# Performance work log

Hardware: AMD Instinct MI355X
Metric: run time of the kernel (lower is better)

Reference implementation:

```python
import jax, jax.numpy as jnp
import numpy as np

DIM = 2048
INTER = 1408
N_EXPERTS = 16
TOP_K = 2
N_SHARED = 2
SHARED_INTER = N_SHARED * INTER  # 2816


def setup_inputs() -> dict:
    key = jax.random.key(0)
    ks = jax.random.split(key, 9)
    s = 0.02
    return {
        "x": jax.random.normal(ks[0], (4, 2048, DIM), dtype=jnp.float32),
        "gate_w": jax.random.normal(ks[1], (N_EXPERTS, DIM), dtype=jnp.float32) * s,
        "w1": jax.random.normal(ks[2], (N_EXPERTS, INTER, DIM), dtype=jnp.float32) * s,
        "w2": jax.random.normal(ks[3], (N_EXPERTS, DIM, INTER), dtype=jnp.float32) * s,
        "w3": jax.random.normal(ks[4], (N_EXPERTS, INTER, DIM), dtype=jnp.float32) * s,
        "sw1": jax.random.normal(ks[5], (SHARED_INTER, DIM), dtype=jnp.float32) * s,
        "sw2": jax.random.normal(ks[6], (DIM, SHARED_INTER), dtype=jnp.float32) * s,
        "sw3": jax.random.normal(ks[7], (SHARED_INTER, DIM), dtype=jnp.float32) * s,
    }


def _swiglu(t, wa, wb, wo):
    # t: [T, d_in]; wa, wb: [d_h, d_in]; wo: [d_out, d_h]
    h = jax.nn.silu(t @ wa.T) * (t @ wb.T)
    return h @ wo.T


def reference(x, gate_w, w1, w2, w3, sw1, sw2, sw3):
    shape = x.shape
    t = x.reshape(-1, DIM)                      # [T, dim]
    scores = jax.nn.softmax(t @ gate_w.T, axis=-1)  # [T, E]
    weights, indices = jax.lax.top_k(scores, TOP_K)  # [T, k] each

    y = jnp.zeros_like(t)
    # Small fixed loop over experts (structurally distinct weights).
    # Per-token combine weight for expert e: sum over top-k slots routed to e
    # (matches y[idx] += expert(x[idx]) * weights[idx, top]; zero weight for
    # unrouted tokens reproduces the counts[i]==0 skip exactly).
    for e in range(N_EXPERTS):
        w_e = jnp.sum(jnp.where(indices == e, weights, 0.0), axis=-1)  # [T]
        y = y + _swiglu(t, w1[e], w3[e], w2[e]) * w_e[:, None]

    z = _swiglu(t, sw1, sw3, sw2)               # shared experts MLP
    return (y + z).reshape(shape)
```

## Files before the change

kernel.cpp:

```cpp
#include <hip/hip_runtime.h>
#include <hip/hip_bf16.h>

#define DIM 2048
#define INTER 1408
#define NEXP 16
#define NTOK 8192
#define SINTER 2816

typedef __attribute__((ext_vector_type(8))) short bf16x8;
typedef __attribute__((ext_vector_type(4))) float f32x4;
typedef __attribute__((ext_vector_type(4))) unsigned short u16x4;
typedef __attribute__((ext_vector_type(8))) unsigned short u16x8;

#define VMCNT(n) asm volatile("s_waitcnt vmcnt(" #n ")" ::: "memory")
#define BARRIER() __builtin_amdgcn_s_barrier()
#define SCHEDB() __builtin_amdgcn_sched_barrier(0)

__device__ __forceinline__ unsigned short f2bf(float f) {
    union { float f; unsigned u; } a; a.f = f;
    unsigned r = a.u + 0x7fffu + ((a.u >> 16) & 1u);
    return (unsigned short)(r >> 16);
}

__device__ __forceinline__ void gload16(const void* g, void* lds) {
    __builtin_amdgcn_global_load_lds(
        (const __attribute__((address_space(1))) void*)g,
        (__attribute__((address_space(3))) void*)lds, 16, 0, 0);
}

__global__ __launch_bounds__(256) void cast_bf16(const float* __restrict__ s,
                                                 unsigned short* __restrict__ d,
                                                 long long n) {
    long long i = ((long long)blockIdx.x * 256 + threadIdx.x) * 8;
    if (i >= n) return;
    float4 a = *(const float4*)(s + i), b = *(const float4*)(s + i + 4);
    u16x8 o = { f2bf(a.x), f2bf(a.y), f2bf(a.z), f2bf(a.w),
                f2bf(b.x), f2bf(b.y), f2bf(b.z), f2bf(b.w) };
    *(u16x8*)(d + i) = o;
}

__global__ __launch_bounds__(256) void gate_topk(
    const float* __restrict__ x, const float* __restrict__ gw,
    unsigned short* __restrict__ xb,
    int* __restrict__ counts, int* __restrict__ toklist, float* __restrict__ tokw) {
    int wave = threadIdx.x >> 6;
    int lane = threadIdx.x & 63;
    int tok  = blockIdx.x * 4 + wave;
    const float* xr = x + (size_t)tok * DIM;
    unsigned short* xbr = xb + (size_t)tok * DIM;

    float part[NEXP];
#pragma unroll
    for (int e = 0; e < NEXP; ++e) part[e] = 0.f;
#pragma unroll
    for (int c = 0; c < DIM / 256; ++c) {
        float4 xv = *(const float4*)(xr + c * 256 + lane * 4);
        u16x4 xo = { f2bf(xv.x), f2bf(xv.y), f2bf(xv.z), f2bf(xv.w) };
        *(u16x4*)(xbr + c * 256 + lane * 4) = xo;
#pragma unroll
        for (int e = 0; e < NEXP; ++e) {
            float4 g = *(const float4*)(gw + e * DIM + c * 256 + lane * 4);
            part[e] += xv.x * g.x + xv.y * g.y + xv.z * g.z + xv.w * g.w;
        }
    }
#pragma unroll
    for (int e = 0; e < NEXP; ++e) {
        float v = part[e];
#pragma unroll
        for (int off = 32; off; off >>= 1) v += __shfl_xor(v, off);
        part[e] = v;
    }
    float mx = part[0];
#pragma unroll
    for (int e = 1; e < NEXP; ++e) mx = fmaxf(mx, part[e]);
    float Z = 0.f;
#pragma unroll
    for (int e = 0; e < NEXP; ++e) Z += expf(part[e] - mx);
    int i1 = 0; float m1 = part[0];
#pragma unroll
    for (int e = 1; e < NEXP; ++e) if (part[e] > m1) { m1 = part[e]; i1 = e; }
    int i2 = -1; float m2 = -1e30f;
#pragma unroll
    for (int e = 0; e < NEXP; ++e) if (e != i1 && part[e] > m2) { m2 = part[e]; i2 = e; }
    if (lane == 0) {
        float w1v = expf(m1 - mx) / Z;
        float w2v = expf(m2 - mx) / Z;
        int p1 = atomicAdd(&counts[i1], 1);
        toklist[i1 * NTOK + p1] = tok; tokw[i1 * NTOK + p1] = w1v;
        int p2 = atomicAdd(&counts[i2], 1);
        toklist[i2 * NTOK + p2] = tok; tokw[i2 * NTOK + p2] = w2v;
    }
}

__global__ void prefix_k(const int* __restrict__ counts, int* __restrict__ base) {
    if (threadIdx.x == 0) {
        int acc = 0;
        for (int e = 0; e < NEXP; ++e) { base[e] = acc; acc += counts[e]; }
        base[16] = acc;
        base[17] = acc + NTOK;
    }
}

__device__ __forceinline__ int swz(int r) { return (r ^ (r >> 2)) & 3; }

__global__ __launch_bounds__(512, 2) void gemm1(
    const unsigned short* __restrict__ xb,
    const unsigned short* __restrict__ w1b, const unsigned short* __restrict__ w3b,
    const unsigned short* __restrict__ sw1b, const unsigned short* __restrict__ sw3b,
    const int* __restrict__ counts, const int* __restrict__ base,
    const int* __restrict__ toklist, unsigned short* __restrict__ hbuf) {
    const int e   = blockIdx.z;
    const int cnt = (e < NEXP) ? counts[e] : NTOK;
    const int m0  = blockIdx.y * 256;
    if (m0 >= cnt) return;
    const int n0  = blockIdx.x * 128;
    const size_t woff = (size_t)((e < NEXP) ? e : e - NEXP) * INTER * DIM;
    const unsigned short* B1 = ((e < NEXP) ? w1b : sw1b) + woff;
    const unsigned short* B3 = ((e < NEXP) ? w3b : sw3b) + woff;
    const int hbase = base[e];
    const int* tl = toklist + e * NTOK;

    __shared__ __attribute__((aligned(16))) unsigned short As[4][8192];
    __shared__ __attribute__((aligned(16))) unsigned short B1s[4][4096];
    __shared__ __attribute__((aligned(16))) unsigned short B3s[4][4096];

    const int tid = threadIdx.x;
    const int w = tid >> 6, l = tid & 63;
    const int wr = w >> 1, wc = w & 1;
    const int lr = l & 15, hi = l >> 4;

    const int row0 = tid >> 2, row1 = row0 + 128;
    const int c0 = (tid & 3) ^ swz(row0);
    int g0 = m0 + row0, g1 = m0 + row1;
    int t0, t1;
    if (e < NEXP) { t0 = (g0 < cnt) ? tl[g0] : 0; t1 = (g1 < cnt) ? tl[g1] : 0; }
    else          { t0 = g0; t1 = g1; }
    const unsigned short* aSrc0 = xb + (size_t)t0 * DIM + c0 * 8;
    const unsigned short* aSrc1 = xb + (size_t)t1 * DIM + c0 * 8;
    const unsigned short* b1Src = B1 + (size_t)(n0 + row0) * DIM + c0 * 8;
    const unsigned short* b3Src = B3 + (size_t)(n0 + row0) * DIM + c0 * 8;

    int aoff[4], boff[4];
#pragma unroll
    for (int m = 0; m < 4; ++m) {
        int r = wr * 64 + m * 16 + lr;
        aoff[m] = r * 64 + ((swz(r) ^ hi) << 4);
    }
#pragma unroll
    for (int n = 0; n < 4; ++n) {
        int r = wc * 64 + n * 16 + lr;
        boff[n] = r * 64 + ((swz(r) ^ hi) << 4);
    }

    f32x4 acc1[4][4], acc3[4][4];
#pragma unroll
    for (int m = 0; m < 4; ++m)
#pragma unroll
        for (int n = 0; n < 4; ++n) {
            acc1[m][n] = (f32x4){0.f, 0.f, 0.f, 0.f};
            acc3[m][n] = (f32x4){0.f, 0.f, 0.f, 0.f};
        }

    const int H = DIM / 32;

    auto STAGE = [&](int hh) {
        int hb = hh & 3;
        int kc = hh * 32;
        gload16(aSrc0 + kc, &As[hb][tid * 8]);
        gload16(aSrc1 + kc, &As[hb][4096 + tid * 8]);
        gload16(b1Src + kc, &B1s[hb][tid * 8]);
        gload16(b3Src + kc, &B3s[hb][tid * 8]);
    };
    auto READF = [&](bf16x8 (&af)[4], bf16x8 (&b1)[4], bf16x8 (&b3)[4], int hh) {
        int hb = hh & 3;
        const char* As_ = (const char*)&As[hb][0];
        const char* B1_ = (const char*)&B1s[hb][0];
        const char* B3_ = (const char*)&B3s[hb][0];
#pragma unroll
        for (int m = 0; m < 4; ++m) af[m] = *(const bf16x8*)(As_ + aoff[m]);
#pragma unroll
        for (int n = 0; n < 4; ++n) {
            b1[n] = *(const bf16x8*)(B1_ + boff[n]);
            b3[n] = *(const bf16x8*)(B3_ + boff[n]);
        }
    };
    auto MMA = [&](bf16x8 (&af)[4], bf16x8 (&b1)[4], bf16x8 (&b3)[4]) {
        __builtin_amdgcn_s_setprio(1);
#pragma unroll
        for (int m = 0; m < 4; ++m)
#pragma unroll
            for (int n = 0; n < 4; ++n) {
                acc1[m][n] = __builtin_amdgcn_mfma_f32_16x16x32_bf16(af[m], b1[n], acc1[m][n], 0, 0, 0);
                acc3[m][n] = __builtin_amdgcn_mfma_f32_16x16x32_bf16(af[m], b3[n], acc3[m][n], 0, 0, 0);
            }
        __builtin_amdgcn_s_setprio(0);
    };

    bf16x8 afA[4], b1A[4], b3A[4], afB[4], b1B[4], b3B[4];

    STAGE(0); STAGE(1); STAGE(2);
    VMCNT(8);
    BARRIER();
    READF(afA, b1A, b3A, 0);

    for (int h = 0; h < H; h += 2) {
        if (h + 3 < H) { STAGE(h + 3); VMCNT(8); }
        else if (h == H - 2) { VMCNT(0); }
        BARRIER();
        READF(afB, b1B, b3B, h + 1);
        SCHEDB();
        MMA(afA, b1A, b3A);
        if (h + 4 < H) { STAGE(h + 4); VMCNT(8); }
        else if (h + 1 == H - 3) { VMCNT(4); }
        BARRIER();
        READF(afA, b1A, b3A, h + 2);
        SCHEDB();
        MMA(afB, b1B, b3B);
    }

#pragma unroll
    for (int m = 0; m < 4; ++m) {
#pragma unroll
        for (int i = 0; i < 4; ++i) {
            int row  = wr * 64 + m * 16 + hi * 4 + i;
            int grow = m0 + row;
            if (grow < cnt) {
                size_t ro = (size_t)(hbase + grow) * INTER;
#pragma unroll
                for (int n = 0; n < 4; ++n) {
                    int col = n0 + wc * 64 + n * 16 + lr;
                    float a = acc1[m][n][i];
                    float hv = a / (1.f + __expf(-a)) * acc3[m][n][i];
                    hbuf[ro + col] = f2bf(hv);
                }
            }
        }
    }
}

__global__ __launch_bounds__(512, 2) void gemm2(
    const unsigned short* __restrict__ hbuf,
    const unsigned short* __restrict__ w2b, const unsigned short* __restrict__ sw2b,
    const int* __restrict__ counts, const int* __restrict__ base,
    const int* __restrict__ toklist, const float* __restrict__ tokw,
    float* __restrict__ out) {
    const int e   = blockIdx.z;
    const int cnt = (e < NEXP) ? counts[e] : NTOK;
    const int m0  = blockIdx.y * 256;
    if (m0 >= cnt) return;
    const int n0  = blockIdx.x * 128;
    const int hbase = base[e];
    const size_t bstride = (e < NEXP) ? INTER : SINTER;
    const unsigned short* Bb = (e < NEXP) ? w2b + (size_t)e * DIM * INTER
                                          : sw2b + (size_t)(e - NEXP) * INTER;

    __shared__ __attribute__((aligned(16))) unsigned short Ah[4][8192];
    __shared__ __attribute__((aligned(16))) unsigned short Bh[4][4096];

    const int tid = threadIdx.x;
    const int w = tid >> 6, l = tid & 63;
    const int wr = w >> 1, wc = w & 1;
    const int lr = l & 15, hi = l >> 4;

    const int row0 = tid >> 2, row1 = row0 + 128;
    const int c0 = (tid & 3) ^ swz(row0);
    const unsigned short* aSrc0 = hbuf + (size_t)(hbase + m0 + row0) * INTER + c0 * 8;
    const unsigned short* aSrc1 = hbuf + (size_t)(hbase + m0 + row1) * INTER + c0 * 8;
    const unsigned short* bSrc  = Bb + (size_t)(n0 + row0) * bstride + c0 * 8;

    int aoff[4], boff[4];
#pragma unroll
    for (int m = 0; m < 4; ++m) {
        int r = wr * 64 + m * 16 + lr;
        aoff[m] = r * 64 + ((swz(r) ^ hi) << 4);
    }
#pragma unroll
    for (int n = 0; n < 4; ++n) {
        int r = wc * 64 + n * 16 + lr;
        boff[n] = r * 64 + ((swz(r) ^ hi) << 4);
    }

    f32x4 acc[4][4];
#pragma unroll
    for (int m = 0; m < 4; ++m)
#pragma unroll
        for (int n = 0; n < 4; ++n) acc[m][n] = (f32x4){0.f, 0.f, 0.f, 0.f};

    const int H = INTER / 32;

    auto STAGE = [&](int hh) {
        int hb = hh & 3;
        int kc = hh * 32;
        gload16(aSrc0 + kc, &Ah[hb][tid * 8]);
        gload16(aSrc1 + kc, &Ah[hb][4096 + tid * 8]);
        gload16(bSrc  + kc, &Bh[hb][tid * 8]);
    };
    auto READF = [&](bf16x8 (&af)[4], bf16x8 (&bf)[4], int hh) {
        int hb = hh & 3;
        const char* A_ = (const char*)&Ah[hb][0];
        const char* B_ = (const char*)&Bh[hb][0];
#pragma unroll
        for (int m = 0; m < 4; ++m) af[m] = *(const bf16x8*)(A_ + aoff[m]);
#pragma unroll
        for (int n = 0; n < 4; ++n) bf[n] = *(const bf16x8*)(B_ + boff[n]);
    };
    auto MMA = [&](bf16x8 (&af)[4], bf16x8 (&bf)[4]) {
        __builtin_amdgcn_s_setprio(1);
#pragma unroll
        for (int m = 0; m < 4; ++m)
#pragma unroll
            for (int n = 0; n < 4; ++n)
                acc[m][n] = __builtin_amdgcn_mfma_f32_16x16x32_bf16(af[m], bf[n], acc[m][n], 0, 0, 0);
        __builtin_amdgcn_s_setprio(0);
    };

    bf16x8 afA[4], bfA[4], afB[4], bfB[4];

    STAGE(0); STAGE(1); STAGE(2);
    VMCNT(6);
    BARRIER();
    READF(afA, bfA, 0);

    for (int h = 0; h < H; h += 2) {
        if (h + 3 < H) { STAGE(h + 3); VMCNT(6); }
        else if (h == H - 2) { VMCNT(0); }
        BARRIER();
        READF(afB, bfB, h + 1);
        SCHEDB();
        MMA(afA, bfA);
        if (h + 4 < H) { STAGE(h + 4); VMCNT(6); }
        else if (h + 1 == H - 3) { VMCNT(3); }
        BARRIER();
        READF(afA, bfA, h + 2);
        SCHEDB();
        MMA(afB, bfB);
    }

#pragma unroll
    for (int m = 0; m < 4; ++m) {
#pragma unroll
        for (int i = 0; i < 4; ++i) {
            int row  = wr * 64 + m * 16 + hi * 4 + i;
            int grow = m0 + row;
            if (grow < cnt) {
                int tok; float wt;
                if (e < NEXP) { tok = toklist[e * NTOK + grow]; wt = tokw[e * NTOK + grow]; }
                else          { tok = grow; wt = 1.f; }
                float* orow = out + (size_t)tok * DIM + n0 + wc * 64 + lr;
#pragma unroll
                for (int n = 0; n < 4; ++n)
                    unsafeAtomicAdd(orow + n * 16, acc[m][n][i] * wt);
            }
        }
    }
}

extern "C" void kernel_launch(void* const* d_in, const int* in_sizes, int n_in,
                              void* d_out, int out_size, void* d_ws, size_t ws_size,
                              hipStream_t stream) {
    const float* x   = (const float*)d_in[0];
    const float* gw  = (const float*)d_in[1];
    const float* w1  = (const float*)d_in[2];
    const float* w2  = (const float*)d_in[3];
    const float* w3  = (const float*)d_in[4];
    const float* sw1 = (const float*)d_in[5];
    const float* sw2 = (const float*)d_in[6];
    const float* sw3 = (const float*)d_in[7];
    float* out = (float*)d_out;

    char* ws = (char*)d_ws;
    int*   counts  = (int*)ws;
    int*   basep   = (int*)(ws + 128);
    int*   toklist = (int*)(ws + 4096);
    float* tokw    = (float*)(ws + 4096 + (size_t)NEXP * NTOK * 4);
    unsigned short* hbuf = (unsigned short*)(ws + (2u << 20));

    const size_t hbytes = (size_t)4 * NTOK * INTER * 2;
    const size_t offx   = (2ull << 20) + hbytes;
    const size_t xbytes = (size_t)NTOK * DIM * 2;
    const size_t offw   = offx + xbytes;
    const size_t wB     = (size_t)NEXP * INTER * DIM * 2;
    const size_t swB    = (size_t)SINTER * DIM * 2;

    unsigned short* xb   = (unsigned short*)(ws + offx);
    unsigned short* w1b  = (unsigned short*)(ws + offw);
    unsigned short* w3b  = (unsigned short*)(ws + offw + wB);
    unsigned short* w2b  = (unsigned short*)(ws + offw + 2 * wB);
    unsigned short* sw1b = (unsigned short*)(ws + offw + 3 * wB);
    unsigned short* sw3b = (unsigned short*)(ws + offw + 3 * wB + swB);
    unsigned short* sw2b = (unsigned short*)(ws + offw + 3 * wB + 2 * swB);

    hipMemsetAsync(counts, 0, 64, stream);
    hipMemsetAsync(d_out, 0, (size_t)out_size * sizeof(float), stream);

    gate_topk<<<NTOK / 4, 256, 0, stream>>>(x, gw, xb, counts, toklist, tokw);
    prefix_k<<<1, 64, 0, stream>>>(counts, basep);

    auto cast = [&](const float* s, unsigned short* d, long long n) {
        cast_bf16<<<(int)((n / 8 + 255) / 256), 256, 0, stream>>>(s, d, n);
    };
    cast(w1, w1b, (long long)NEXP * INTER * DIM);
    cast(w3, w3b, (long long)NEXP * INTER * DIM);
    cast(w2, w2b, (long long)NEXP * INTER * DIM);
    cast(sw1, sw1b, (long long)SINTER * DIM);
    cast(sw3, sw3b, (long long)SINTER * DIM);
    cast(sw2, sw2b, (long long)SINTER * DIM);

    gemm1<<<dim3(INTER / 128, NTOK / 256, 18), 512, 0, stream>>>(
        xb, w1b, w3b, sw1b, sw3b, counts, basep, toklist, hbuf);
    gemm2<<<dim3(DIM / 128, NTOK / 256, 18), 512, 0, stream>>>(
        hbuf, w2b, sw2b, counts, basep, toklist, tokw, out);
}
```

Baseline: 1.444 ms.

## Simplify GEMM pipelines to single-buffered register loop with prefetch distance two

Both GEMM main loops drop the unrolled A/B register double-buffering and the sched barriers. Each iteration now loads fragments from LDS, issues the global-to-LDS stage two tiles ahead (previously three), waits, then runs the MFMAs with the n loop outermost and the w1 and w3 products issued separately. This lowers register pressure and lets the compiler schedule freely, but exposes LDS read latency before the MFMAs and reduces prefetch depth. The w2 and sw2 weight casts now launch after gemm1 instead of before it.

```diff
diff --git a/kernel.cpp b/kernel.cpp
--- a/kernel.cpp
+++ b/kernel.cpp
@@ -14,7 +14,6 @@
 
 #define VMCNT(n) asm volatile("s_waitcnt vmcnt(" #n ")" ::: "memory")
 #define BARRIER() __builtin_amdgcn_s_barrier()
-#define SCHEDB() __builtin_amdgcn_sched_barrier(0)
 
 __device__ __forceinline__ unsigned short f2bf(float f) {
     union { float f; unsigned u; } a; a.f = f;
@@ -125,9 +124,9 @@
     __shared__ __attribute__((aligned(16))) unsigned short B3s[4][4096];
 
     const int tid = threadIdx.x;
-    const int w = tid >> 6, l = tid & 63;
+    const int w = tid >> 6, lu = tid & 63;
     const int wr = w >> 1, wc = w & 1;
-    const int lr = l & 15, hi = l >> 4;
+    const int lr = lu & 15, hi = lu >> 4;
 
     const int row0 = tid >> 2, row1 = row0 + 128;
     const int c0 = (tid & 3) ^ swz(row0);
@@ -171,51 +170,39 @@
         gload16(b1Src + kc, &B1s[hb][tid * 8]);
         gload16(b3Src + kc, &B3s[hb][tid * 8]);
     };
-    auto READF = [&](bf16x8 (&af)[4], bf16x8 (&b1)[4], bf16x8 (&b3)[4], int hh) {
-        int hb = hh & 3;
+
+    STAGE(0); STAGE(1);
+    VMCNT(4);
+    BARRIER();
+
+    for (int h = 0; h < H; ++h) {
+        const int hb = h & 3;
         const char* As_ = (const char*)&As[hb][0];
         const char* B1_ = (const char*)&B1s[hb][0];
         const char* B3_ = (const char*)&B3s[hb][0];
+        bf16x8 af[4], b1f[4], b3f[4];
 #pragma unroll
         for (int m = 0; m < 4; ++m) af[m] = *(const bf16x8*)(As_ + aoff[m]);
 #pragma unroll
         for (int n = 0; n < 4; ++n) {
-            b1[n] = *(const bf16x8*)(B1_ + boff[n]);
-            b3[n] = *(const bf16x8*)(B3_ + boff[n]);
-        }
-    };
-    auto MMA = [&](bf16x8 (&af)[4], bf16x8 (&b1)[4], bf16x8 (&b3)[4]) {
+            b1f[n] = *(const bf16x8*)(B1_ + boff[n]);
+            b3f[n] = *(const bf16x8*)(B3_ + boff[n]);
+        }
+        if (h + 2 < H) { STAGE(h + 2); VMCNT(4); }
+        else           { VMCNT(0); }
+        BARRIER();
         __builtin_amdgcn_s_setprio(1);
 #pragma unroll
-        for (int m = 0; m < 4; ++m)
-#pragma unroll
-            for (int n = 0; n < 4; ++n) {
-                acc1[m][n] = __builtin_amdgcn_mfma_f32_16x16x32_bf16(af[m], b1[n], acc1[m][n], 0, 0, 0);
-                acc3[m][n] = __builtin_amdgcn_mfma_f32_16x16x32_bf16(af[m], b3[n], acc3[m][n], 0, 0, 0);
-            }
+        for (int n = 0; n < 4; ++n)
+#pragma unroll
+            for (int m = 0; m < 4; ++m)
+                acc1[m][n] = __builtin_amdgcn_mfma_f32_16x16x32_bf16(af[m], b1f[n], acc1[m][n], 0, 0, 0);
+#pragma unroll
+        for (int n = 0; n < 4; ++n)
+#pragma unroll
+            for (int m = 0; m < 4; ++m)
+                acc3[m][n] = __builtin_amdgcn_mfma_f32_16x16x32_bf16(af[m], b3f[n], acc3[m][n], 0, 0, 0);
         __builtin_amdgcn_s_setprio(0);
-    };
-
-    bf16x8 afA[4], b1A[4], b3A[4], afB[4], b1B[4], b3B[4];
-
-    STAGE(0); STAGE(1); STAGE(2);
-    VMCNT(8);
-    BARRIER();
-    READF(afA, b1A, b3A, 0);
-
-    for (int h = 0; h < H; h += 2) {
-        if (h + 3 < H) { STAGE(h + 3); VMCNT(8); }
-        else if (h == H - 2) { VMCNT(0); }
-        BARRIER();
-        READF(afB, b1B, b3B, h + 1);
-        SCHEDB();
-        MMA(afA, b1A, b3A);
-        if (h + 4 < H) { STAGE(h + 4); VMCNT(8); }
-        else if (h + 1 == H - 3) { VMCNT(4); }
-        BARRIER();
-        READF(afA, b1A, b3A, h + 2);
-        SCHEDB();
-        MMA(afB, b1B, b3B);
     }
 
 #pragma unroll
@@ -258,9 +245,9 @@
     __shared__ __attribute__((aligned(16))) unsigned short Bh[4][4096];
 
     const int tid = threadIdx.x;
-    const int w = tid >> 6, l = tid & 63;
+    const int w = tid >> 6, lu = tid & 63;
     const int wr = w >> 1, wc = w & 1;
-    const int lr = l & 15, hi = l >> 4;
+    const int lr = lu & 15, hi = lu >> 4;
 
     const int row0 = tid >> 2, row1 = row0 + 128;
     const int c0 = (tid & 3) ^ swz(row0);
@@ -295,45 +282,30 @@
         gload16(aSrc1 + kc, &Ah[hb][4096 + tid * 8]);
         gload16(bSrc  + kc, &Bh[hb][tid * 8]);
     };
-    auto READF = [&](bf16x8 (&af)[4], bf16x8 (&bf)[4], int hh) {
-        int hb = hh & 3;
+
+    STAGE(0); STAGE(1);
+    VMCNT(3);
+    BARRIER();
+
+    for (int h = 0; h < H; ++h) {
+        const int hb = h & 3;
         const char* A_ = (const char*)&Ah[hb][0];
         const char* B_ = (const char*)&Bh[hb][0];
+        bf16x8 af[4], bf[4];
 #pragma unroll
         for (int m = 0; m < 4; ++m) af[m] = *(const bf16x8*)(A_ + aoff[m]);
 #pragma unroll
         for (int n = 0; n < 4; ++n) bf[n] = *(const bf16x8*)(B_ + boff[n]);
-    };
-    auto MMA = [&](bf16x8 (&af)[4], bf16x8 (&bf)[4]) {
+        if (h + 2 < H) { STAGE(h + 2); VMCNT(3); }
+        else           { VMCNT(0); }
+        BARRIER();
         __builtin_amdgcn_s_setprio(1);
 #pragma unroll
-        for (int m = 0; m < 4; ++m)
-#pragma unroll
-            for (int n = 0; n < 4; ++n)
+        for (int n = 0; n < 4; ++n)
+#pragma unroll
+            for (int m = 0; m < 4; ++m)
                 acc[m][n] = __builtin_amdgcn_mfma_f32_16x16x32_bf16(af[m], bf[n], acc[m][n], 0, 0, 0);
         __builtin_amdgcn_s_setprio(0);
-    };
-
-    bf16x8 afA[4], bfA[4], afB[4], bfB[4];
-
-    STAGE(0); STAGE(1); STAGE(2);
-    VMCNT(6);
-    BARRIER();
-    READF(afA, bfA, 0);
-
-    for (int h = 0; h < H; h += 2) {
-        if (h + 3 < H) { STAGE(h + 3); VMCNT(6); }
-        else if (h == H - 2) { VMCNT(0); }
-        BARRIER();
-        READF(afB, bfB, h + 1);
-        SCHEDB();
-        MMA(afA, bfA);
-        if (h + 4 < H) { STAGE(h + 4); VMCNT(6); }
-        else if (h + 1 == H - 3) { VMCNT(3); }
-        BARRIER();
-        READF(afA, bfA, h + 2);
-        SCHEDB();
-        MMA(afB, bfB);
     }
 
 #pragma unroll
@@ -401,13 +373,15 @@
     };
     cast(w1, w1b, (long long)NEXP * INTER * DIM);
     cast(w3, w3b, (long long)NEXP * INTER * DIM);
-    cast(w2, w2b, (long long)NEXP * INTER * DIM);
     cast(sw1, sw1b, (long long)SINTER * DIM);
     cast(sw3, sw3b, (long long)SINTER * DIM);
-    cast(sw2, sw2b, (long long)SINTER * DIM);
 
     gemm1<<<dim3(INTER / 128, NTOK / 256, 18), 512, 0, stream>>>(
         xb, w1b, w3b, sw1b, sw3b, counts, basep, toklist, hbuf);
+
+    cast(w2, w2b, (long long)NEXP * INTER * DIM);
+    cast(sw2, sw2b, (long long)SINTER * DIM);
+
     gemm2<<<dim3(DIM / 128, NTOK / 256, 18), 512, 0, stream>>>(
         hbuf, w2b, sw2b, counts, basep, toklist, tokw, out);
 }
```

After: 1.345 ms. 6.8% less time.
